# Performance work log

Measured on AMD Instinct MI355X. Metric: run time of the kernel, lower is better.

Reference implementation:

```python
import jax, jax.numpy as jnp
import numpy as np
from jax import lax

PERM = (0, 1, 4, 5, 2, 3)  # swap the two (H,W) spatial pairs
DN = ('NCHWXY', 'OIHWXY', 'NCHWXY')  # 4 spatial dims -> native 4D conv


def conv4d(x, w, b):
    # x: [B,Ci,S,S,S,S], w: [Co,Ci,k1,k1,k2,k2], 'SAME' padding as in ANCNet Conv4d
    y = lax.conv_general_dilated(x, w, window_strides=(1, 1, 1, 1),
                                 padding='SAME', dimension_numbers=DN)
    return y + b[None, :, None, None, None, None]


def setup_inputs() -> dict:
    key = jax.random.key(0)
    ks = jax.random.split(key, 10)
    B, S = 2, 25
    def w_init(k, shape):
        fan_in = shape[1] * np.prod(shape[2:])
        return jax.random.normal(k, shape, jnp.float32) * (1.0 / np.sqrt(fan_in))
    return {
        'x': jax.random.normal(ks[0], (B, 1, S, S, S, S), jnp.float32),
        'w0': w_init(ks[1], (8, 1, 3, 3, 5, 5)),   'b0': jnp.zeros((8,), jnp.float32),
        'w1': w_init(ks[2], (8, 1, 5, 5, 5, 5)),   'b1': jnp.zeros((8,), jnp.float32),
        'w2a': w_init(ks[3], (16, 16, 5, 5, 5, 5)), 'b2a': jnp.zeros((16,), jnp.float32),
        'w2b': w_init(ks[4], (1, 16, 5, 5, 5, 5)),  'b2b': jnp.zeros((1,), jnp.float32),
    }


def reference(x, w0, b0, w1, b1, w2a, b2a, w2b, b2b):
    relu = jax.nn.relu
    conv0 = lambda t: relu(conv4d(t, w0, b0))
    conv1 = lambda t: relu(conv4d(t, w1, b1))
    conv2 = lambda t: relu(conv4d(relu(conv4d(t, w2a, b2a)), w2b, b2b))
    sym = lambda f, t: f(t) + jnp.transpose(f(jnp.transpose(t, PERM)), PERM)
    x0 = sym(conv0, x)
    x1 = sym(conv1, x)
    h = jnp.concatenate((x0, x1), axis=1)  # [B,16,S,S,S,S]
    return sym(conv2, h)
```

## Files before the change

kernel.cpp:

```cpp
#include <hip/hip_runtime.h>

#define S 25
#define PLANE 625
#define VOL 390625
#define CLn 12500000

typedef __attribute__((ext_vector_type(8))) short short8;
typedef __attribute__((ext_vector_type(4))) float f32x4;
typedef __attribute__((ext_vector_type(4))) unsigned short us4;
typedef __attribute__((ext_vector_type(4))) unsigned int u32x4;

__device__ __forceinline__ unsigned short f2bf(float f) {
    unsigned int u = __float_as_uint(f);
    u += 0x7fffu + ((u >> 16) & 1u);
    return (unsigned short)(u >> 16);
}

__device__ __forceinline__ int xcd_swz(int orig, int nwg) {
    int q = nwg >> 3, r = nwg & 7;
    int x = orig & 7, lid = orig >> 3;
    return (x < r ? x * (q + 1) : r * (q + 1) + (x - r) * q) + lid;
}

__device__ __forceinline__ int nxt_kd(int kd, int d0, int d1) {
    #pragma unroll 1
    for (++kd; kd < 25; ++kd) {
        int kd0 = kd / 5, kd1 = kd - kd0 * 5;
        int e0 = d0 + kd0 - 2, e1 = d1 + kd1 - 2;
        if (e0 >= 0 && e0 < S && e1 >= 0 && e1 < S) return kd;
    }
    return 25;
}

__device__ __forceinline__ int nxt_uv(int uv, int D0, int D1) {
    #pragma unroll 1
    for (++uv; uv < 36; ++uv) {
        int u = uv / 6, v6 = uv - u * 6;
        int e0 = D0 - 2 + u, e1 = D1 - 2 + v6;
        if (e0 >= 0 && e0 < S && e1 >= 0 && e1 < S) return uv;
    }
    return 36;
}

__global__ __launch_bounds__(256) void prep_weights(
    const float* __restrict__ w2a, const float* __restrict__ w2b,
    const float* __restrict__ w0, const float* __restrict__ w1,
    unsigned short* __restrict__ wbig, unsigned short* __restrict__ wl1,
    unsigned short* __restrict__ wp2)
{
    int idx = blockIdx.x * 256 + threadIdx.x;
    if (idx < 332800) {
        int k = idx & 31;
        int co = (idx >> 5) & 15;
        int tile = (idx >> 9) & 1;
        int rem = idx >> 10;
        int pr = rem % 13, kd01 = rem / 13;
        int t = 2 * pr + (k >> 4), ci = k & 15;
        float v = 0.f;
        if (t <= 24)
            v = (tile == 0) ? w2a[(co * 16 + ci) * 625 + kd01 * 25 + t]
                            : w2a[(co * 16 + ci) * 625 + t * 25 + kd01];
        wbig[idx] = f2bf(v);
    } else if (idx < 332800 + 25600) {
        int j = idx - 332800;
        int k = j & 31;
        int row = (j >> 5) & 15;
        int tile = (j >> 9) & 1;
        int kd01 = j >> 10;
        int kd0 = kd01 / 5, kd1 = kd01 - kd0 * 5;
        float v = 0.f;
        if (k < 25) {
            int t = k, kd2 = t / 5, kd3 = t - kd2 * 5;
            if (tile == 0) {
                v = (row < 8) ? w1[row * 625 + kd0 * 125 + kd1 * 25 + t]
                              : w1[(row - 8) * 625 + t * 25 + kd01];
            } else {
                if (row < 8) {
                    if (kd0 >= 1 && kd0 <= 3 && kd1 >= 1 && kd1 <= 3)
                        v = w0[((row * 3 + (kd0 - 1)) * 3 + (kd1 - 1)) * 25 + t];
                } else {
                    if (kd2 >= 1 && kd2 <= 3 && kd3 >= 1 && kd3 <= 3)
                        v = w0[(row - 8) * 225 + ((kd2 - 1) * 3 + (kd3 - 1)) * 25 + kd01];
                }
            }
        }
        wl1[j] = f2bf(v);
    } else if (idx < 332800 + 25600 + 230400) {
        int j = idx - 358400;
        int k = j & 31;
        int row = (j >> 5) & 7;
        int rem = j >> 8;
        int t = rem % 25, uv = rem / 25;
        int u = uv / 6, v6 = uv - u * 6;
        int path = row & 1, o = row >> 1;
        int py = o >> 1, px = o & 1;
        int kd0 = u - py, kd1 = v6 - px;
        float v = 0.f;
        if (kd0 >= 0 && kd0 < 5 && kd1 >= 0 && kd1 < 5) {
            int ci = k & 15;
            if (path == 0 && k < 16)
                v = w2b[ci * 625 + (kd0 * 5 + kd1) * 25 + t];
            else if (path == 1 && k >= 16)
                v = w2b[ci * 625 + t * 25 + kd0 * 5 + kd1];
        }
        wp2[j] = f2bf(v);
    }
}

__global__ __launch_bounds__(256) void layer1_mfma(
    const float* __restrict__ x, const unsigned short* __restrict__ wl1,
    const float* __restrict__ b0, const float* __restrict__ b1,
    unsigned short* __restrict__ hbf)
{
    __shared__ __align__(16) unsigned short pl[29 * 32];
    const int blk = blockIdx.x;
    const int b = blk / PLANE;
    const int d01 = blk - b * PLANE;
    const int d0 = d01 / S, d1 = d01 - d0 * S;
    const int tid = threadIdx.x;
    const int l = tid & 63, w = tid >> 6;
    const int col = l & 15, kq = l >> 4;

    int off[8];
    #pragma unroll
    for (int j = 0; j < 8; ++j) {
        int t = kq * 8 + j; if (t > 24) t = 24;
        int t5 = t / 5;
        off[j] = t5 * 32 + (t - t5 * 5);
    }
    int rb[10];
    #pragma unroll
    for (int g = 0; g < 10; ++g) {
        int n = (w * 10 + g) * 16 + col; if (n > 624) n = 624;
        int d2 = n / 25;
        rb[g] = d2 * 32 + (n - d2 * 25);
    }

    f32x4 acc0[10], acc1[10];
    #pragma unroll
    for (int g = 0; g < 10; ++g) {
        acc0[g] = (f32x4){0.f, 0.f, 0.f, 0.f};
        acc1[g] = (f32x4){0.f, 0.f, 0.f, 0.f};
    }

    const float* xb = x + (size_t)b * VOL;

    #pragma unroll 1
    for (int kd01 = 0; kd01 < 25; ++kd01) {
        const int kd0 = kd01 / 5, kd1 = kd01 - kd0 * 5;
        const int e0 = d0 + kd0 - 2, e1 = d1 + kd1 - 2;
        if (e0 < 0 || e0 >= S || e1 < 0 || e1 >= S) continue;
        __syncthreads();
        {
            const float* sp = xb + (e0 * 25 + e1) * 625;
            for (int i = tid; i < 841; i += 256) {
                int r = i / 29, c = i - r * 29;
                float v = 0.f;
                if (r >= 2 && r <= 26 && c >= 2 && c <= 26)
                    v = sp[(r - 2) * 25 + (c - 2)];
                pl[r * 32 + c] = f2bf(v);
            }
        }
        __syncthreads();
        const unsigned short* wp = wl1 + kd01 * 1024;
        short8 a0 = *(const short8*)(wp + col * 32 + kq * 8);
        short8 a1 = *(const short8*)(wp + 512 + col * 32 + kq * 8);
        #pragma unroll
        for (int g = 0; g < 10; ++g) {
            short8 bf;
            #pragma unroll
            for (int j = 0; j < 8; ++j)
                bf[j] = (short)pl[rb[g] + off[j]];
            acc0[g] = __builtin_amdgcn_mfma_f32_16x16x32_bf16(a0, bf, acc0[g], 0, 0, 0);
            acc1[g] = __builtin_amdgcn_mfma_f32_16x16x32_bf16(a1, bf, acc1[g], 0, 0, 0);
        }
    }

    const int ch = (kq & 1) * 4;
    float bi1[4], bi0[4];
    #pragma unroll
    for (int r = 0; r < 4; ++r) { bi1[r] = b1[ch + r]; bi0[r] = b0[ch + r]; }
    const bool lo = (kq < 2);
    const size_t obase = (size_t)(b * 625 + d01) * 625;
    #pragma unroll
    for (int g = 0; g < 10; ++g) {
        int n = (w * 10 + g) * 16 + col;
        float r0[4], r1[4];
        #pragma unroll
        for (int r = 0; r < 4; ++r) {
            r0[r] = fmaxf(acc0[g][r] + bi1[r], 0.f);
            r1[r] = fmaxf(acc1[g][r] + bi0[r], 0.f);
        }
        us4 u0, u1;
        #pragma unroll
        for (int r = 0; r < 4; ++r) {
            float p0 = __shfl_xor(r0[r], 32, 64);
            float p1 = __shfl_xor(r1[r], 32, 64);
            u0[r] = f2bf(r0[r] + p0);
            u1[r] = f2bf(r1[r] + p1);
        }
        if (lo && n < 625) {
            *(us4*)&hbf[(obase + n) * 16 + 8 + ch] = u0;
            *(us4*)&hbf[(obase + n) * 16 + ch]     = u1;
        }
    }
}

__global__ __launch_bounds__(256, 3) void conv_mfma(
    const unsigned short* __restrict__ in, const unsigned short* __restrict__ wq,
    const float* __restrict__ bias,
    unsigned short* __restrict__ gA, unsigned short* __restrict__ gB)
{
    __shared__ __align__(16) unsigned short pl[841 * 24];
    const int blk = xcd_swz(blockIdx.x, 1250);
    const int b = blk / PLANE;
    const int d01 = blk - b * PLANE;
    const int d0 = d01 / S, d1 = d01 - d0 * S;
    const int tid = threadIdx.x;
    const int l = tid & 63, w = tid >> 6;
    const int tp = l >> 5;
    const int kq = (l >> 4) & 3;
    const int h8 = (kq & 1) * 8;
    const int col = l & 15;

    int ofsG[7], ofsL[7]; bool ok[7];
    #pragma unroll
    for (int j = 0; j < 7; ++j) {
        int cid = tid + j * 256;
        int r = cid / 58, w8 = cid - r * 58;
        int c = w8 >> 1, hh = w8 & 1;
        ok[j] = (cid < 1682) && (r >= 2 && r <= 26 && c >= 2 && c <= 26);
        ofsG[j] = ((r - 2) * 25 + (c - 2)) * 16 + hh * 8;
        ofsL[j] = (r * 29 + c) * 24 + hh * 8;
    }

    int rb24[10];
    #pragma unroll
    for (int g = 0; g < 10; ++g) {
        int n = (w * 10 + g) * 16 + col;
        if (n > 624) n = 624;
        int d2 = n / 25, d3 = n - d2 * 25;
        rb24[g] = (d2 * 29 + d3) * 24;
    }

    f32x4 acc[10][2];
    #pragma unroll
    for (int g = 0; g < 10; ++g) {
        acc[g][0] = (f32x4){0.f, 0.f, 0.f, 0.f};
        acc[g][1] = (f32x4){0.f, 0.f, 0.f, 0.f};
    }

    const unsigned short* inb = in + (size_t)b * 625 * 10000;

    u32x4 stg[7];
    int kd_cur = nxt_kd(-1, d0, d1);
    {
        int kd0 = kd_cur / 5, kd1 = kd_cur - kd0 * 5;
        const unsigned short* sb = inb + (size_t)((d0 + kd0 - 2) * 25 + (d1 + kd1 - 2)) * 10000;
        #pragma unroll
        for (int j = 0; j < 7; ++j) {
            u32x4 z = {0u, 0u, 0u, 0u};
            if (ok[j]) z = *(const u32x4*)(sb + ofsG[j]);
            stg[j] = z;
        }
    }

    #pragma unroll 1
    while (kd_cur < 25) {
        const int kd01 = kd_cur;
        const int kd_nxt = nxt_kd(kd_cur, d0, d1);
        __syncthreads();
        #pragma unroll
        for (int j = 0; j < 7; ++j)
            if (j < 6 || tid < 146) *(u32x4*)&pl[ofsL[j]] = stg[j];
        __syncthreads();
        if (kd_nxt < 25) {
            int kd0 = kd_nxt / 5, kd1 = kd_nxt - kd0 * 5;
            const unsigned short* sb = inb + (size_t)((d0 + kd0 - 2) * 25 + (d1 + kd1 - 2)) * 10000;
            #pragma unroll
            for (int j = 0; j < 7; ++j) {
                u32x4 z = {0u, 0u, 0u, 0u};
                if (ok[j]) z = *(const u32x4*)(sb + ofsG[j]);
                stg[j] = z;
            }
        }

        #pragma unroll 1
        for (int pr = 0; pr < 13; ++pr) {
            const unsigned short* wp = wq + (size_t)kd01 * 13312 + pr * 1024;
            short8 a0 = *(const short8*)(wp + col * 32 + kq * 8);
            short8 a1 = *(const short8*)(wp + 512 + col * 32 + kq * 8);
            int t = 2 * pr + tp;
            if (t > 24) t = 24;
            int t5 = t / 5;
            int aofs = (t5 * 29 + (t - t5 * 5)) * 24 + h8;
            #pragma unroll
            for (int g = 0; g < 10; ++g) {
                short8 bfrag = *(const short8*)&pl[rb24[g] + aofs];
                acc[g][0] = __builtin_amdgcn_mfma_f32_16x16x32_bf16(a0, bfrag, acc[g][0], 0, 0, 0);
                acc[g][1] = __builtin_amdgcn_mfma_f32_16x16x32_bf16(a1, bfrag, acc[g][1], 0, 0, 0);
            }
        }
        kd_cur = kd_nxt;
    }

    const int cob = kq * 4;
    float bi[4];
    #pragma unroll
    for (int r = 0; r < 4; ++r) bi[r] = bias[cob + r];
    #pragma unroll
    for (int g = 0; g < 10; ++g) {
        int n = (w * 10 + g) * 16 + col;
        if (n < 625) {
            size_t ob = ((size_t)(b * 625 + d01) * 625 + n) * 16 + cob;
            us4 ua, ub;
            #pragma unroll
            for (int r = 0; r < 4; ++r) {
                ua[r] = f2bf(fmaxf(acc[g][0][r] + bi[r], 0.f));
                ub[r] = f2bf(fmaxf(acc[g][1][r] + bi[r], 0.f));
            }
            *(us4*)&gA[ob] = ua;
            *(us4*)&gB[ob] = ub;
        }
    }
}

__global__ __launch_bounds__(512, 4) void convc_v2(
    const unsigned short* __restrict__ gA,
    const unsigned short* __restrict__ wp2, const float* __restrict__ b2b,
    float* __restrict__ outp)
{
    __shared__ __align__(16) unsigned short pl[841 * 36];
    const int blk = xcd_swz(blockIdx.x, 338);
    const int b = blk / 169;
    const int rem = blk - b * 169;
    const int D0 = (rem / 13) * 2, D1 = (rem % 13) * 2;
    const int tid = threadIdx.x;
    const int l = tid & 63, wv = tid >> 6;
    const int col = l & 15, kq = l >> 4;

    int ofsG[7], ofsL[7]; bool ok[7];
    #pragma unroll
    for (int j = 0; j < 7; ++j) {
        int cid = tid + j * 512;
        int p = cid >> 2, q = cid & 3;
        int r = p / 29, c = p - r * 29;
        ok[j] = (cid < 3364) && (r >= 2 && r <= 26 && c >= 2 && c <= 26);
        ofsG[j] = (q >> 1) * CLn + ((r - 2) * 25 + (c - 2)) * 16 + (q & 1) * 8;
        ofsL[j] = p * 36 + (q >> 1) * 16 + (q & 1) * 8;
    }

    int rb[5];
    #pragma unroll
    for (int g = 0; g < 5; ++g) {
        int n = (wv * 5 + g) * 16 + col; if (n > 624) n = 624;
        int d2 = n / 25;
        rb[g] = (d2 * 29 + (n - d2 * 25)) * 36;
    }

    f32x4 acc[5];
    #pragma unroll
    for (int g = 0; g < 5; ++g) acc[g] = (f32x4){0.f, 0.f, 0.f, 0.f};

    const unsigned short* gAb = gA + (size_t)b * 625 * 10000;

    u32x4 stg[7];
    int uv_cur = nxt_uv(-1, D0, D1);
    {
        int u = uv_cur / 6, v6 = uv_cur - u * 6;
        const unsigned short* sb = gAb + (size_t)((D0 - 2 + u) * 25 + (D1 - 2 + v6)) * 10000;
        #pragma unroll
        for (int j = 0; j < 7; ++j) {
            u32x4 z = {0u, 0u, 0u, 0u};
            if (ok[j]) z = *(const u32x4*)(sb + ofsG[j]);
            stg[j] = z;
        }
    }

    #pragma unroll 1
    while (uv_cur < 36) {
        const int uvc = uv_cur;
        const int uv_nxt = nxt_uv(uv_cur, D0, D1);
        __syncthreads();
        #pragma unroll
        for (int j = 0; j < 7; ++j)
            if (j < 6 || tid < 292) *(u32x4*)&pl[ofsL[j]] = stg[j];
        __syncthreads();
        if (uv_nxt < 36) {
            int u = uv_nxt / 6, v6 = uv_nxt - u * 6;
            const unsigned short* sb = gAb + (size_t)((D0 - 2 + u) * 25 + (D1 - 2 + v6)) * 10000;
            #pragma unroll
            for (int j = 0; j < 7; ++j) {
                u32x4 z = {0u, 0u, 0u, 0u};
                if (ok[j]) z = *(const u32x4*)(sb + ofsG[j]);
                stg[j] = z;
            }
        }

        const unsigned short* wbase = wp2 + uvc * 25 * 256;
        #pragma unroll 1
        for (int t = 0; t < 25; ++t) {
            const int t5 = t / 5;
            const int toff = (t5 * 29 + (t - t5 * 5)) * 36;
            short8 a = {0, 0, 0, 0, 0, 0, 0, 0};
            if (col < 8)
                a = *(const short8*)(wbase + (t * 8 + col) * 32 + kq * 8);
            #pragma unroll
            for (int g = 0; g < 5; ++g) {
                short8 bf = *(const short8*)&pl[rb[g] + toff + kq * 8];
                acc[g] = __builtin_amdgcn_mfma_f32_16x16x32_bf16(a, bf, acc[g], 0, 0, 0);
            }
        }
        uv_cur = uv_nxt;
    }

    if (kq < 2) {
        const float bv = b2b[0];
        #pragma unroll
        for (int g = 0; g < 5; ++g) {
            int n = (wv * 5 + g) * 16 + col;
            if (n < 625) {
                #pragma unroll
                for (int oo = 0; oo < 2; ++oo) {
                    int o = kq * 2 + oo;
                    int d0 = D0 + (o >> 1), d1 = D1 + (o & 1);
                    if (d0 < S && d1 < S) {
                        float vA = acc[g][oo * 2], vB = acc[g][oo * 2 + 1];
                        outp[((size_t)b * 625 + d0 * 25 + d1) * 625 + n] =
                            fmaxf(vA + bv, 0.f) + fmaxf(vB + bv, 0.f);
                    }
                }
            }
        }
    }
}

extern "C" void kernel_launch(void* const* d_in, const int* in_sizes, int n_in,
                              void* d_out, int out_size, void* d_ws, size_t ws_size,
                              hipStream_t stream) {
    const float* x   = (const float*)d_in[0];
    const float* w0  = (const float*)d_in[1];
    const float* b0  = (const float*)d_in[2];
    const float* w1  = (const float*)d_in[3];
    const float* b1  = (const float*)d_in[4];
    const float* w2a = (const float*)d_in[5];
    const float* b2a = (const float*)d_in[6];
    const float* w2b = (const float*)d_in[7];
    const float* b2b = (const float*)d_in[8];
    float* out = (float*)d_out;

    unsigned short* hbf  = (unsigned short*)d_ws;
    unsigned short* gA   = hbf + CLn;
    unsigned short* gB   = gA + CLn;
    unsigned short* wbig = gB + CLn;
    unsigned short* wl1  = wbig + 332800;
    unsigned short* wp2  = wl1 + 25600;
    if (ws_size < ((size_t)3 * CLn + 332800 + 25600 + 230400) * sizeof(unsigned short)) return;

    const int nblk = 2 * PLANE;

    prep_weights<<<2300, 256, 0, stream>>>(w2a, w2b, w0, w1, wbig, wl1, wp2);
    layer1_mfma<<<nblk, 256, 0, stream>>>(x, wl1, b0, b1, hbf);
    conv_mfma<<<nblk, 256, 0, stream>>>(hbf, wbig, b2a, gA, gB);
    convc_v2<<<338, 512, 0, stream>>>(gA, wp2, b2b, out);
}
```

Baseline: 998.6 us.

## Share input planes across adjacent output pairs in 16-channel conv and final conv

The middle conv now has each block compute two adjacent d1 output planes with 512 threads. Each staged input plane in LDS feeds both outputs through shifted weight slices, which cuts global plane loads per output. The final conv moves from 2x2 to 2x4 output tiles split into two halves of the n dimension, using all 16 MFMA rows instead of 8 and halving the LDS plane size. The cost is more accumulator registers, fewer and larger blocks (650 and 364), and a larger repacked weight buffer.

```diff
diff --git a/kernel.cpp b/kernel.cpp
--- a/kernel.cpp
+++ b/kernel.cpp
@@ -22,31 +22,21 @@
     return (x < r ? x * (q + 1) : r * (q + 1) + (x - r) * q) + lid;
 }
 
-__device__ __forceinline__ int nxt_kd(int kd, int d0, int d1) {
+__device__ __forceinline__ int nxt_w(int uv, int U, int V, int b0, int b1) {
     #pragma unroll 1
-    for (++kd; kd < 25; ++kd) {
-        int kd0 = kd / 5, kd1 = kd - kd0 * 5;
-        int e0 = d0 + kd0 - 2, e1 = d1 + kd1 - 2;
-        if (e0 >= 0 && e0 < S && e1 >= 0 && e1 < S) return kd;
-    }
-    return 25;
-}
-
-__device__ __forceinline__ int nxt_uv(int uv, int D0, int D1) {
-    #pragma unroll 1
-    for (++uv; uv < 36; ++uv) {
-        int u = uv / 6, v6 = uv - u * 6;
-        int e0 = D0 - 2 + u, e1 = D1 - 2 + v6;
+    for (++uv; uv < U * V; ++uv) {
+        int u = uv / V, v = uv - u * V;
+        int e0 = b0 + u, e1 = b1 + v;
         if (e0 >= 0 && e0 < S && e1 >= 0 && e1 < S) return uv;
     }
-    return 36;
+    return U * V;
 }
 
 __global__ __launch_bounds__(256) void prep_weights(
     const float* __restrict__ w2a, const float* __restrict__ w2b,
     const float* __restrict__ w0, const float* __restrict__ w1,
     unsigned short* __restrict__ wbig, unsigned short* __restrict__ wl1,
-    unsigned short* __restrict__ wp2)
+    unsigned short* __restrict__ wcp)
 {
     int idx = blockIdx.x * 256 + threadIdx.x;
     if (idx < 332800) {
@@ -61,7 +51,7 @@
             v = (tile == 0) ? w2a[(co * 16 + ci) * 625 + kd01 * 25 + t]
                             : w2a[(co * 16 + ci) * 625 + t * 25 + kd01];
         wbig[idx] = f2bf(v);
-    } else if (idx < 332800 + 25600) {
+    } else if (idx < 358400) {
         int j = idx - 332800;
         int k = j & 31;
         int row = (j >> 5) & 15;
@@ -85,16 +75,16 @@
             }
         }
         wl1[j] = f2bf(v);
-    } else if (idx < 332800 + 25600 + 230400) {
+    } else if (idx < 358400 + 614400) {
         int j = idx - 358400;
         int k = j & 31;
-        int row = (j >> 5) & 7;
-        int rem = j >> 8;
+        int row = (j >> 5) & 15;
+        int rem = j >> 9;
         int t = rem % 25, uv = rem / 25;
-        int u = uv / 6, v6 = uv - u * 6;
+        int u = uv >> 3, v8 = uv & 7;
         int path = row & 1, o = row >> 1;
-        int py = o >> 1, px = o & 1;
-        int kd0 = u - py, kd1 = v6 - px;
+        int py = o >> 2, px = o & 3;
+        int kd0 = u - py, kd1 = v8 - px;
         float v = 0.f;
         if (kd0 >= 0 && kd0 < 5 && kd1 >= 0 && kd1 < 5) {
             int ci = k & 15;
@@ -103,7 +93,7 @@
             else if (path == 1 && k >= 16)
                 v = w2b[ci * 625 + t * 25 + kd0 * 5 + kd1];
         }
-        wp2[j] = f2bf(v);
+        wcp[j] = f2bf(v);
     }
 }
 
@@ -206,16 +196,18 @@
     }
 }
 
-__global__ __launch_bounds__(256, 3) void conv_mfma(
+__global__ __launch_bounds__(512, 2) void conv_mfma_p2(
     const unsigned short* __restrict__ in, const unsigned short* __restrict__ wq,
     const float* __restrict__ bias,
     unsigned short* __restrict__ gA, unsigned short* __restrict__ gB)
 {
     __shared__ __align__(16) unsigned short pl[841 * 24];
-    const int blk = xcd_swz(blockIdx.x, 1250);
-    const int b = blk / PLANE;
-    const int d01 = blk - b * PLANE;
-    const int d0 = d01 / S, d1 = d01 - d0 * S;
+    const int blk = xcd_swz(blockIdx.x, 650);
+    const int b = blk / 325;
+    const int rem = blk - b * 325;
+    const int d0 = rem / 13, dp = rem - d0 * 13;
+    const int d1a = dp * 2;
+    const bool haveB = (d1a + 1 < S);
     const int tid = threadIdx.x;
     const int l = tid & 63, w = tid >> 6;
     const int tp = l >> 5;
@@ -223,10 +215,10 @@
     const int h8 = (kq & 1) * 8;
     const int col = l & 15;
 
-    int ofsG[7], ofsL[7]; bool ok[7];
-    #pragma unroll
-    for (int j = 0; j < 7; ++j) {
-        int cid = tid + j * 256;
+    int ofsG[4], ofsL[4]; bool ok[4];
+    #pragma unroll
+    for (int j = 0; j < 4; ++j) {
+        int cid = tid + j * 512;
         int r = cid / 58, w8 = cid - r * 58;
         int c = w8 >> 1, hh = w8 & 1;
         ok[j] = (cid < 1682) && (r >= 2 && r <= 26 && c >= 2 && c <= 26);
@@ -234,31 +226,33 @@
         ofsL[j] = (r * 29 + c) * 24 + hh * 8;
     }
 
-    int rb24[10];
-    #pragma unroll
-    for (int g = 0; g < 10; ++g) {
-        int n = (w * 10 + g) * 16 + col;
+    int rb24[5];
+    #pragma unroll
+    for (int g = 0; g < 5; ++g) {
+        int n = (w * 5 + g) * 16 + col;
         if (n > 624) n = 624;
         int d2 = n / 25, d3 = n - d2 * 25;
         rb24[g] = (d2 * 29 + d3) * 24;
     }
 
-    f32x4 acc[10][2];
-    #pragma unroll
-    for (int g = 0; g < 10; ++g) {
-        acc[g][0] = (f32x4){0.f, 0.f, 0.f, 0.f};
-        acc[g][1] = (f32x4){0.f, 0.f, 0.f, 0.f};
-    }
-
-    const unsigned short* inb = in + (size_t)b * 625 * 10000;
-
-    u32x4 stg[7];
-    int kd_cur = nxt_kd(-1, d0, d1);
+    f32x4 acc[5][2][2];
+    #pragma unroll
+    for (int g = 0; g < 5; ++g)
+        #pragma unroll
+        for (int p = 0; p < 2; ++p) {
+            acc[g][p][0] = (f32x4){0.f, 0.f, 0.f, 0.f};
+            acc[g][p][1] = (f32x4){0.f, 0.f, 0.f, 0.f};
+        }
+
+    const unsigned short* inb = in + (size_t)b * 6250000;
+
+    u32x4 stg[4];
+    int uv_cur = nxt_w(-1, 5, 6, d0 - 2, d1a - 2);
     {
-        int kd0 = kd_cur / 5, kd1 = kd_cur - kd0 * 5;
-        const unsigned short* sb = inb + (size_t)((d0 + kd0 - 2) * 25 + (d1 + kd1 - 2)) * 10000;
-        #pragma unroll
-        for (int j = 0; j < 7; ++j) {
+        int u = uv_cur / 6, v = uv_cur - u * 6;
+        const unsigned short* sb = inb + (size_t)((d0 + u - 2) * 25 + (d1a + v - 2)) * 10000;
+        #pragma unroll
+        for (int j = 0; j < 4; ++j) {
             u32x4 z = {0u, 0u, 0u, 0u};
             if (ok[j]) z = *(const u32x4*)(sb + ofsG[j]);
             stg[j] = z;
@@ -266,42 +260,60 @@
     }
 
     #pragma unroll 1
-    while (kd_cur < 25) {
-        const int kd01 = kd_cur;
-        const int kd_nxt = nxt_kd(kd_cur, d0, d1);
-        __syncthreads();
-        #pragma unroll
-        for (int j = 0; j < 7; ++j)
-            if (j < 6 || tid < 146) *(u32x4*)&pl[ofsL[j]] = stg[j];
-        __syncthreads();
-        if (kd_nxt < 25) {
-            int kd0 = kd_nxt / 5, kd1 = kd_nxt - kd0 * 5;
-            const unsigned short* sb = inb + (size_t)((d0 + kd0 - 2) * 25 + (d1 + kd1 - 2)) * 10000;
-            #pragma unroll
-            for (int j = 0; j < 7; ++j) {
+    while (uv_cur < 30) {
+        const int u = uv_cur / 6, v = uv_cur - u * 6;
+        const int uv_nxt = nxt_w(uv_cur, 5, 6, d0 - 2, d1a - 2);
+        __syncthreads();
+        #pragma unroll
+        for (int j = 0; j < 4; ++j)
+            if (j < 3 || tid < 146) *(u32x4*)&pl[ofsL[j]] = stg[j];
+        __syncthreads();
+        if (uv_nxt < 30) {
+            int un = uv_nxt / 6, vn = uv_nxt - un * 6;
+            const unsigned short* sb = inb + (size_t)((d0 + un - 2) * 25 + (d1a + vn - 2)) * 10000;
+            #pragma unroll
+            for (int j = 0; j < 4; ++j) {
                 u32x4 z = {0u, 0u, 0u, 0u};
                 if (ok[j]) z = *(const u32x4*)(sb + ofsG[j]);
                 stg[j] = z;
             }
         }
 
+        const bool vp0 = (v < 5);
+        const bool vp1 = (v >= 1) && haveB;
+        const unsigned short* wp0 = wq + (size_t)(u * 5 + v) * 13312;
+        const unsigned short* wp1 = wq + (size_t)(u * 5 + v - 1) * 13312;
+
         #pragma unroll 1
         for (int pr = 0; pr < 13; ++pr) {
-            const unsigned short* wp = wq + (size_t)kd01 * 13312 + pr * 1024;
-            short8 a0 = *(const short8*)(wp + col * 32 + kq * 8);
-            short8 a1 = *(const short8*)(wp + 512 + col * 32 + kq * 8);
             int t = 2 * pr + tp;
             if (t > 24) t = 24;
             int t5 = t / 5;
             int aofs = (t5 * 29 + (t - t5 * 5)) * 24 + h8;
-            #pragma unroll
-            for (int g = 0; g < 10; ++g) {
-                short8 bfrag = *(const short8*)&pl[rb24[g] + aofs];
-                acc[g][0] = __builtin_amdgcn_mfma_f32_16x16x32_bf16(a0, bfrag, acc[g][0], 0, 0, 0);
-                acc[g][1] = __builtin_amdgcn_mfma_f32_16x16x32_bf16(a1, bfrag, acc[g][1], 0, 0, 0);
-            }
-        }
-        kd_cur = kd_nxt;
+            short8 bf[5];
+            #pragma unroll
+            for (int g = 0; g < 5; ++g)
+                bf[g] = *(const short8*)&pl[rb24[g] + aofs];
+            if (vp0) {
+                short8 a0 = *(const short8*)(wp0 + pr * 1024 + col * 32 + kq * 8);
+                short8 a1 = *(const short8*)(wp0 + pr * 1024 + 512 + col * 32 + kq * 8);
+                #pragma unroll
+                for (int g = 0; g < 5; ++g) {
+                    acc[g][0][0] = __builtin_amdgcn_mfma_f32_16x16x32_bf16(a0, bf[g], acc[g][0][0], 0, 0, 0);
+                    acc[g][0][1] = __builtin_amdgcn_mfma_f32_16x16x32_bf16(a1, bf[g], acc[g][0][1], 0, 0, 0);
+                }
+            }
+            if (vp1) {
+                short8 a0 = *(const short8*)(wp1 + pr * 1024 + col * 32 + kq * 8);
+                short8 a1 = *(const short8*)(wp1 + pr * 1024 + 512 + col * 32 + kq * 8);
+                #pragma unroll
+                for (int g = 0; g < 5; ++g) {
+                    acc[g][1][0] = __builtin_amdgcn_mfma_f32_16x16x32_bf16(a0, bf[g], acc[g][1][0], 0, 0, 0);
+                    acc[g][1][1] = __builtin_amdgcn_mfma_f32_16x16x32_bf16(a1, bf[g], acc[g][1][1], 0, 0, 0);
+                }
+            }
+        }
+        uv_cur = uv_nxt;
     }
 
     const int cob = kq * 4;
@@ -309,68 +321,78 @@
     #pragma unroll
     for (int r = 0; r < 4; ++r) bi[r] = bias[cob + r];
     #pragma unroll
-    for (int g = 0; g < 10; ++g) {
-        int n = (w * 10 + g) * 16 + col;
-        if (n < 625) {
-            size_t ob = ((size_t)(b * 625 + d01) * 625 + n) * 16 + cob;
-            us4 ua, ub;
-            #pragma unroll
-            for (int r = 0; r < 4; ++r) {
-                ua[r] = f2bf(fmaxf(acc[g][0][r] + bi[r], 0.f));
-                ub[r] = f2bf(fmaxf(acc[g][1][r] + bi[r], 0.f));
-            }
-            *(us4*)&gA[ob] = ua;
-            *(us4*)&gB[ob] = ub;
-        }
-    }
-}
-
-__global__ __launch_bounds__(512, 4) void convc_v2(
+    for (int p = 0; p < 2; ++p) {
+        if (p == 1 && !haveB) break;
+        const size_t obP = ((size_t)b * 625 + d0 * 25 + d1a + p) * 625;
+        #pragma unroll
+        for (int g = 0; g < 5; ++g) {
+            int n = (w * 5 + g) * 16 + col;
+            if (n < 625) {
+                size_t ob = (obP + n) * 16 + cob;
+                us4 ua, ub;
+                #pragma unroll
+                for (int r = 0; r < 4; ++r) {
+                    ua[r] = f2bf(fmaxf(acc[g][p][0][r] + bi[r], 0.f));
+                    ub[r] = f2bf(fmaxf(acc[g][p][1][r] + bi[r], 0.f));
+                }
+                *(us4*)&gA[ob] = ua;
+                *(us4*)&gB[ob] = ub;
+            }
+        }
+    }
+}
+
+__global__ __launch_bounds__(256, 3) void convc_v3(
     const unsigned short* __restrict__ gA,
-    const unsigned short* __restrict__ wp2, const float* __restrict__ b2b,
+    const unsigned short* __restrict__ wcp, const float* __restrict__ b2b,
     float* __restrict__ outp)
 {
-    __shared__ __align__(16) unsigned short pl[841 * 36];
-    const int blk = xcd_swz(blockIdx.x, 338);
-    const int b = blk / 169;
-    const int rem = blk - b * 169;
-    const int D0 = (rem / 13) * 2, D1 = (rem % 13) * 2;
+    __shared__ __align__(16) unsigned short pl[493 * 36];
+    const int blk = xcd_swz(blockIdx.x, 364);
+    const int h = blk & 1;
+    const int geo = blk >> 1;
+    const int b = geo / 91;
+    const int g91 = geo - b * 91;
+    const int t0 = g91 / 7, t1 = g91 - t0 * 7;
+    const int D0 = t0 * 2, D1 = t1 * 4;
+    const int r0 = h ? 10 : -2;
     const int tid = threadIdx.x;
-    const int l = tid & 63, wv = tid >> 6;
+    const int l = tid & 63, w = tid >> 6;
     const int col = l & 15, kq = l >> 4;
 
-    int ofsG[7], ofsL[7]; bool ok[7];
-    #pragma unroll
-    for (int j = 0; j < 7; ++j) {
-        int cid = tid + j * 512;
+    int ofsG[8], ofsL[8]; bool ok[8];
+    #pragma unroll
+    for (int j = 0; j < 8; ++j) {
+        int cid = tid + j * 256;
         int p = cid >> 2, q = cid & 3;
         int r = p / 29, c = p - r * 29;
-        ok[j] = (cid < 3364) && (r >= 2 && r <= 26 && c >= 2 && c <= 26);
-        ofsG[j] = (q >> 1) * CLn + ((r - 2) * 25 + (c - 2)) * 16 + (q & 1) * 8;
-        ofsL[j] = p * 36 + (q >> 1) * 16 + (q & 1) * 8;
+        int d2e = r + r0, d3e = c - 2;
+        ok[j] = (cid < 1972) && (d2e >= 0 && d2e < S) && (d3e >= 0 && d3e < S);
+        ofsG[j] = (q >> 1) * CLn + (d2e * 25 + d3e) * 16 + (q & 1) * 8;
+        ofsL[j] = p * 36 + q * 8;
     }
 
     int rb[5];
     #pragma unroll
     for (int g = 0; g < 5; ++g) {
-        int n = (wv * 5 + g) * 16 + col; if (n > 624) n = 624;
+        int n = h * 320 + (w * 5 + g) * 16 + col; if (n > 624) n = 624;
         int d2 = n / 25;
-        rb[g] = (d2 * 29 + (n - d2 * 25)) * 36;
+        rb[g] = ((d2 - (h ? 12 : 0)) * 29 + (n - d2 * 25)) * 36;
     }
 
     f32x4 acc[5];
     #pragma unroll
     for (int g = 0; g < 5; ++g) acc[g] = (f32x4){0.f, 0.f, 0.f, 0.f};
 
-    const unsigned short* gAb = gA + (size_t)b * 625 * 10000;
-
-    u32x4 stg[7];
-    int uv_cur = nxt_uv(-1, D0, D1);
+    const unsigned short* gAb = gA + (size_t)b * 6250000;
+
+    u32x4 stg[8];
+    int uv_cur = nxt_w(-1, 6, 8, D0 - 2, D1 - 2);
     {
-        int u = uv_cur / 6, v6 = uv_cur - u * 6;
-        const unsigned short* sb = gAb + (size_t)((D0 - 2 + u) * 25 + (D1 - 2 + v6)) * 10000;
-        #pragma unroll
-        for (int j = 0; j < 7; ++j) {
+        int u = uv_cur >> 3, v = uv_cur & 7;
+        const unsigned short* sb = gAb + (size_t)((D0 - 2 + u) * 25 + (D1 - 2 + v)) * 10000;
+        #pragma unroll
+        for (int j = 0; j < 8; ++j) {
             u32x4 z = {0u, 0u, 0u, 0u};
             if (ok[j]) z = *(const u32x4*)(sb + ofsG[j]);
             stg[j] = z;
@@ -378,33 +400,31 @@
     }
 
     #pragma unroll 1
-    while (uv_cur < 36) {
+    while (uv_cur < 48) {
         const int uvc = uv_cur;
-        const int uv_nxt = nxt_uv(uv_cur, D0, D1);
-        __syncthreads();
-        #pragma unroll
-        for (int j = 0; j < 7; ++j)
-            if (j < 6 || tid < 292) *(u32x4*)&pl[ofsL[j]] = stg[j];
-        __syncthreads();
-        if (uv_nxt < 36) {
-            int u = uv_nxt / 6, v6 = uv_nxt - u * 6;
-            const unsigned short* sb = gAb + (size_t)((D0 - 2 + u) * 25 + (D1 - 2 + v6)) * 10000;
-            #pragma unroll
-            for (int j = 0; j < 7; ++j) {
+        const int uv_nxt = nxt_w(uv_cur, 6, 8, D0 - 2, D1 - 2);
+        __syncthreads();
+        #pragma unroll
+        for (int j = 0; j < 8; ++j)
+            if (j < 7 || tid < 180) *(u32x4*)&pl[ofsL[j]] = stg[j];
+        __syncthreads();
+        if (uv_nxt < 48) {
+            int u = uv_nxt >> 3, v = uv_nxt & 7;
+            const unsigned short* sb = gAb + (size_t)((D0 - 2 + u) * 25 + (D1 - 2 + v)) * 10000;
+            #pragma unroll
+            for (int j = 0; j < 8; ++j) {
                 u32x4 z = {0u, 0u, 0u, 0u};
                 if (ok[j]) z = *(const u32x4*)(sb + ofsG[j]);
                 stg[j] = z;
             }
         }
 
-        const unsigned short* wbase = wp2 + uvc * 25 * 256;
+        const unsigned short* wbase = wcp + (size_t)uvc * 12800;
         #pragma unroll 1
         for (int t = 0; t < 25; ++t) {
             const int t5 = t / 5;
             const int toff = (t5 * 29 + (t - t5 * 5)) * 36;
-            short8 a = {0, 0, 0, 0, 0, 0, 0, 0};
-            if (col < 8)
-                a = *(const short8*)(wbase + (t * 8 + col) * 32 + kq * 8);
+            short8 a = *(const short8*)(wbase + (t * 16 + col) * 32 + kq * 8);
             #pragma unroll
             for (int g = 0; g < 5; ++g) {
                 short8 bf = *(const short8*)&pl[rb[g] + toff + kq * 8];
@@ -414,21 +434,19 @@
         uv_cur = uv_nxt;
     }
 
-    if (kq < 2) {
-        const float bv = b2b[0];
-        #pragma unroll
-        for (int g = 0; g < 5; ++g) {
-            int n = (wv * 5 + g) * 16 + col;
-            if (n < 625) {
-                #pragma unroll
-                for (int oo = 0; oo < 2; ++oo) {
-                    int o = kq * 2 + oo;
-                    int d0 = D0 + (o >> 1), d1 = D1 + (o & 1);
-                    if (d0 < S && d1 < S) {
-                        float vA = acc[g][oo * 2], vB = acc[g][oo * 2 + 1];
-                        outp[((size_t)b * 625 + d0 * 25 + d1) * 625 + n] =
-                            fmaxf(vA + bv, 0.f) + fmaxf(vB + bv, 0.f);
-                    }
+    const float bv = b2b[0];
+    #pragma unroll
+    for (int g = 0; g < 5; ++g) {
+        int n = h * 320 + (w * 5 + g) * 16 + col;
+        if (n < 625) {
+            #pragma unroll
+            for (int r2 = 0; r2 < 2; ++r2) {
+                int o = kq * 2 + r2;
+                int d0 = D0 + (o >> 2), d1 = D1 + (o & 3);
+                if (d0 < S && d1 < S) {
+                    float vA = acc[g][r2 * 2], vB = acc[g][r2 * 2 + 1];
+                    outp[((size_t)b * 625 + d0 * 25 + d1) * 625 + n] =
+                        fmaxf(vA + bv, 0.f) + fmaxf(vB + bv, 0.f);
                 }
             }
         }
@@ -454,13 +472,11 @@
     unsigned short* gB   = gA + CLn;
     unsigned short* wbig = gB + CLn;
     unsigned short* wl1  = wbig + 332800;
-    unsigned short* wp2  = wl1 + 25600;
-    if (ws_size < ((size_t)3 * CLn + 332800 + 25600 + 230400) * sizeof(unsigned short)) return;
-
-    const int nblk = 2 * PLANE;
-
-    prep_weights<<<2300, 256, 0, stream>>>(w2a, w2b, w0, w1, wbig, wl1, wp2);
-    layer1_mfma<<<nblk, 256, 0, stream>>>(x, wl1, b0, b1, hbf);
-    conv_mfma<<<nblk, 256, 0, stream>>>(hbf, wbig, b2a, gA, gB);
-    convc_v2<<<338, 512, 0, stream>>>(gA, wp2, b2b, out);
-}
+    unsigned short* wcp  = wl1 + 25600;
+    if (ws_size < ((size_t)3 * CLn + 332800 + 25600 + 614400) * sizeof(unsigned short)) return;
+
+    prep_weights<<<3800, 256, 0, stream>>>(w2a, w2b, w0, w1, wbig, wl1, wcp);
+    layer1_mfma<<<1250, 256, 0, stream>>>(x, wl1, b0, b1, hbf);
+    conv_mfma_p2<<<650, 512, 0, stream>>>(hbf, wbig, b2a, gA, gB);
+    convc_v3<<<364, 256, 0, stream>>>(gA, wcp, b2b, out);
+}
```

Result: slower. 1.059 ms (+6.1%).
